# Optimization experiments

Measured on AMD Instinct MI355X. Metric: run time of the kernel, lower is better.

The kernel has to match this reference:

```python
import jax, jax.numpy as jnp
import numpy as np

D_MODEL = 1024
D_STATE = 16
EPS = 1e-5


def _layernorm(x, g, b):
    mu = x.mean(-1, keepdims=True)
    xc = x - mu
    var = (xc * xc).mean(-1, keepdims=True)
    return xc * jax.lax.rsqrt(var + EPS) * g + b


def setup_inputs() -> dict:
    key = jax.random.key(0)
    ks = jax.random.split(key, 10)
    B, L, d, n = 8, 1024, D_MODEL, D_STATE
    s = 1.0 / np.sqrt(d)
    return {
        "x": jax.random.normal(ks[0], (B, L, d), jnp.float32),
        "h_prev": jnp.zeros((B, d * n), jnp.float32),
        "ln_g": jnp.ones((d,), jnp.float32),
        "ln_b": jnp.zeros((d,), jnp.float32),
        "W_ig": jax.random.uniform(ks[1], (2 * d, d), jnp.float32, -s, s),
        "W_dt": jax.random.uniform(ks[2], (d, d), jnp.float32, -s, s),
        "b_dt": jax.random.uniform(ks[3], (d,), jnp.float32, -s, s),
        "A_log": jax.random.uniform(ks[4], (d, n), jnp.float32, -3.0, -1.0),
        "W_B": jax.random.uniform(ks[5], (n, d), jnp.float32, -s, s),
        "W_C": jax.random.uniform(ks[6], (n, d), jnp.float32, -s, s),
        "D": jnp.ones((d,), jnp.float32),
        "W_out": jax.random.uniform(ks[7], (d, d), jnp.float32, -s, s),
    }


def reference(x, h_prev, ln_g, ln_b, W_ig, W_dt, b_dt, A_log, W_B, W_C, D, W_out):
    Bsz, L, d = x.shape
    n = A_log.shape[1]
    x_norm = _layernorm(x, ln_g, ln_b)
    x_proj = jnp.einsum('bld,ed->ble', x_norm, W_ig)  # [B,L,2d]
    x_in, z = x_proj[..., :d], x_proj[..., d:]
    dt = jax.nn.softplus(jnp.einsum('bld,ed->ble', x_in, W_dt) + b_dt)  # [B,L,d]
    A = -jnp.exp(A_log)  # [d,n]
    B_t = jnp.einsum('bld,nd->bln', x_in, W_B)  # [B,L,n]
    C_t = jnp.einsum('bld,nd->bln', x_in, W_C)  # [B,L,n]
    h0 = h_prev.reshape(Bsz, d, n)

    def step(h, inp):
        dt_t, xin_t, Bt_t, Ct_t = inp  # [B,d],[B,d],[B,n],[B,n]
        dA = jnp.exp(dt_t[..., None] * A)                      # [B,d,n]
        h = dA * h + (dt_t * xin_t)[..., None] * Bt_t[:, None, :]
        y_t = (h * Ct_t[:, None, :]).sum(-1)                   # [B,d]
        return h, y_t

    xs = (jnp.swapaxes(dt, 0, 1), jnp.swapaxes(x_in, 0, 1),
          jnp.swapaxes(B_t, 0, 1), jnp.swapaxes(C_t, 0, 1))
    h_final, y = jax.lax.scan(step, h0, xs)
    y = jnp.swapaxes(y, 0, 1)  # [B,L,d]
    ssm_out = y * jax.nn.silu(z) + x_in * D
    out = jnp.einsum('bld,ed->ble', ssm_out, W_out)
    return (x + out, h_final.reshape(Bsz, -1))
```

## Files before the change

kernel.cpp:

```cpp
#include <hip/hip_runtime.h>
#include <hip/hip_bf16.h>
#include <math.h>

#define DM 1024
#define NS 16
#define BSZ 8
#define LSEQ 1024
#define MROWS (BSZ*LSEQ)
#define CH 32

typedef __bf16 bf16;
typedef bf16 bf16x8 __attribute__((ext_vector_type(8)));
typedef bf16 bf16x4 __attribute__((ext_vector_type(4)));
typedef float f32x4 __attribute__((ext_vector_type(4)));
typedef unsigned int u32;
typedef unsigned short u16;

__device__ __forceinline__ void async16(const void* g, void* l) {
  __builtin_amdgcn_global_load_lds((const __attribute__((address_space(1))) void*)g,
                                   (__attribute__((address_space(3))) void*)l,
                                   16, 0, 0);
}

__device__ __forceinline__ float bflo(u32 u) { return __builtin_bit_cast(float, (u32)(u << 16)); }
__device__ __forceinline__ float bfhi(u32 u) { return __builtin_bit_cast(float, (u32)(u & 0xffff0000u)); }

template <int CTRL>
__device__ __forceinline__ float dpp_add(float v) {
  int x = __builtin_amdgcn_update_dpp(0, __builtin_bit_cast(int, v), CTRL, 0xf, 0xf, true);
  return v + __builtin_bit_cast(float, x);
}
__device__ __forceinline__ float row_reduce16(float p) {
  p = dpp_add<0x121>(p);
  p = dpp_add<0x122>(p);
  p = dpp_add<0x124>(p);
  p = dpp_add<0x128>(p);
  return p;
}

__global__ void cast_f2b(const float* __restrict__ s, bf16* __restrict__ d, int n4) {
  int i = blockIdx.x * 256 + threadIdx.x;
  if (i < n4) {
    float4 v = ((const float4*)s)[i];
    bf16x4 o;
    o.x = (bf16)v.x; o.y = (bf16)v.y; o.z = (bf16)v.z; o.w = (bf16)v.w;
    *(bf16x4*)(d + 4 * (size_t)i) = o;
  }
}

__global__ void transpose_cast(const float* __restrict__ src, bf16* __restrict__ dst) {
  __shared__ float tile[64][65];
  const int bk = blockIdx.x * 64;
  const int bd = blockIdx.y * 64;
  const int t = threadIdx.x;
  const int c4 = t & 15;
  const int r0 = t >> 4;
#pragma unroll
  for (int p = 0; p < 4; ++p) {
    int r = r0 + p * 16;
    float4 v = *(const float4*)(src + (size_t)(bd + r) * 1024 + bk + c4 * 4);
    tile[r][c4 * 4 + 0] = v.x;
    tile[r][c4 * 4 + 1] = v.y;
    tile[r][c4 * 4 + 2] = v.z;
    tile[r][c4 * 4 + 3] = v.w;
  }
  __syncthreads();
#pragma unroll
  for (int p = 0; p < 4; ++p) {
    int r = r0 + p * 16;
    bf16x4 o;
    o.x = (bf16)tile[c4 * 4 + 0][r];
    o.y = (bf16)tile[c4 * 4 + 1][r];
    o.z = (bf16)tile[c4 * 4 + 2][r];
    o.w = (bf16)tile[c4 * 4 + 3][r];
    *(bf16x4*)(dst + (size_t)(bk + r) * 1024 + bd + c4 * 4) = o;
  }
}

__global__ void ln_kernel(const float* __restrict__ x, const float* __restrict__ g,
                          const float* __restrict__ b, bf16* __restrict__ out) {
  const size_t row = blockIdx.x;
  const int t = threadIdx.x;
  float4 v = ((const float4*)(x + row * DM))[t];
  float s = v.x + v.y + v.z + v.w;
  float s2 = v.x*v.x + v.y*v.y + v.z*v.z + v.w*v.w;
#pragma unroll
  for (int m = 1; m < 64; m <<= 1) { s += __shfl_xor(s, m, 64); s2 += __shfl_xor(s2, m, 64); }
  __shared__ float red[8];
  int wave = t >> 6, lane = t & 63;
  if (lane == 0) { red[wave] = s; red[4 + wave] = s2; }
  __syncthreads();
  s  = red[0] + red[1] + red[2] + red[3];
  s2 = red[4] + red[5] + red[6] + red[7];
  float mu  = s * (1.f / DM);
  float var = s2 * (1.f / DM) - mu * mu;
  float inv = rsqrtf(var + 1e-5f);
  float4 gg = ((const float4*)g)[t];
  float4 bb = ((const float4*)b)[t];
  bf16x4 o;
  o.x = (bf16)((v.x - mu) * inv * gg.x + bb.x);
  o.y = (bf16)((v.y - mu) * inv * gg.y + bb.y);
  o.z = (bf16)((v.z - mu) * inv * gg.z + bb.z);
  o.w = (bf16)((v.w - mu) * inv * gg.w + bb.w);
  *(bf16x4*)(out + row * DM + t * 4) = o;
}

template <int EPI, bool SWZ>
__global__ __launch_bounds__(256)
void gemm_bf16(const bf16* __restrict__ A, const bf16* __restrict__ W, int K,
               float* __restrict__ out_f, bf16* __restrict__ out_b,
               u16* __restrict__ out_u1, u16* __restrict__ out_u2,
               const float* __restrict__ aux,
               float* __restrict__ out_f3, float* __restrict__ out_f4) {
  __shared__ bf16 As[2][128 * 32];
  __shared__ bf16 Bs[2][128 * 32];
  int tx, ty;
  if (SWZ) {
    int g = blockIdx.x;
    int xcd = g & 7, slot = g >> 3;
    tx = slot >> 3;
    ty = xcd * 8 + (slot & 7);
  } else {
    tx = blockIdx.x; ty = blockIdx.y;
  }
  const int tid  = threadIdx.x;
  const int wave = tid >> 6, lane = tid & 63;
  const int lr = lane & 15, quad = lane >> 4;
  const size_t arow = (size_t)ty * 128;
  const size_t brow = (size_t)tx * 128;
  f32x4 acc[4][4] = {};

  const int srl  = lane >> 2;
  const int kg   = lane & 3;
  const int srow = wave * 32 + srl;
  const int skc  = (kg ^ ((srl >> 1) & 3)) * 8;
  const bf16* ag = A + (arow + srow) * (size_t)K + skc;
  const bf16* wg = W + (brow + srow) * (size_t)K + skc;
  bf16* asl0 = &As[0][wave * 32 * 32];
  bf16* asl1 = &As[1][wave * 32 * 32];
  bf16* bsl0 = &Bs[0][wave * 32 * 32];
  bf16* bsl1 = &Bs[1][wave * 32 * 32];

  const int rk = (quad ^ ((lr >> 1) & 3)) * 8;

  for (int k0 = 0; k0 < K; k0 += 64) {
    async16(ag + k0,                       asl0);
    async16(ag + (size_t)16 * K + k0,      asl0 + 16 * 32);
    async16(ag + k0 + 32,                  asl1);
    async16(ag + (size_t)16 * K + k0 + 32, asl1 + 16 * 32);
    async16(wg + k0,                       bsl0);
    async16(wg + (size_t)16 * K + k0,      bsl0 + 16 * 32);
    async16(wg + k0 + 32,                  bsl1);
    async16(wg + (size_t)16 * K + k0 + 32, bsl1 + 16 * 32);
    __syncthreads();
#pragma unroll
    for (int kh = 0; kh < 2; ++kh) {
      const bf16* ap = &As[kh][(((wave >> 1) * 64) + lr) * 32 + rk];
      const bf16* bp = &Bs[kh][(((wave & 1) * 64) + lr) * 32 + rk];
      bf16x8 af[4], bfr[4];
#pragma unroll
      for (int i = 0; i < 4; ++i) af[i] = *(const bf16x8*)(ap + i * 16 * 32);
#pragma unroll
      for (int j = 0; j < 4; ++j) bfr[j] = *(const bf16x8*)(bp + j * 16 * 32);
#pragma unroll
      for (int i = 0; i < 4; ++i)
#pragma unroll
        for (int j = 0; j < 4; ++j)
          acc[i][j] = __builtin_amdgcn_mfma_f32_16x16x32_bf16(af[i], bfr[j], acc[i][j], 0, 0, 0);
    }
    __syncthreads();
  }

  const size_t mbase = arow + (wave >> 1) * 64;
  const size_t nbase = brow + (wave & 1) * 64;
  if (EPI == 0) {
    if (nbase < DM) {
#pragma unroll
      for (int i = 0; i < 4; ++i)
#pragma unroll
        for (int j = 0; j < 4; ++j)
#pragma unroll
          for (int r = 0; r < 4; ++r) {
            size_t m = mbase + i * 16 + quad * 4 + r;
            size_t n = nbase + j * 16 + lr;
            out_u1[m * DM + n] = __builtin_bit_cast(u16, (bf16)acc[i][j][r]);
          }
    } else if (nbase < 2 * DM) {
#pragma unroll
      for (int i = 0; i < 4; ++i)
#pragma unroll
        for (int j = 0; j < 4; ++j)
#pragma unroll
          for (int r = 0; r < 4; ++r) {
            size_t m = mbase + i * 16 + quad * 4 + r;
            size_t n = nbase - DM + j * 16 + lr;
            out_b[m * DM + n] = (bf16)acc[i][j][r];
          }
    } else if (nbase < 3 * DM) {
#pragma unroll
      for (int i = 0; i < 4; ++i)
#pragma unroll
        for (int j = 0; j < 4; ++j)
#pragma unroll
          for (int r = 0; r < 4; ++r) {
            size_t m = mbase + i * 16 + quad * 4 + r;
            size_t n = nbase - 2 * DM + j * 16 + lr;
            float tt = acc[i][j][r] + aux[n];
            float sp = (tt > 20.f) ? tt : __logf(1.f + __expf(tt));
            out_u2[m * DM + n] = __builtin_bit_cast(u16, (bf16)sp);
          }
    } else if (nbase < 3 * DM + 2 * NS) {
#pragma unroll
      for (int i = 0; i < 4; ++i)
#pragma unroll
        for (int r = 0; r < 4; ++r) {
          size_t m = mbase + i * 16 + quad * 4 + r;
          out_f3[m * NS + lr] = acc[i][0][r];
          out_f4[m * NS + lr] = acc[i][1][r];
        }
    }
  } else {
#pragma unroll
    for (int i = 0; i < 4; ++i)
#pragma unroll
      for (int j = 0; j < 4; ++j)
#pragma unroll
        for (int r = 0; r < 4; ++r) {
          size_t m = mbase + i * 16 + quad * 4 + r;
          size_t n = nbase + j * 16 + lr;
          float v = acc[i][j][r];
          if (EPI == 2) {
            out_f[m * DM + n] = v + aux[m * DM + n];
          } else {
            out_b[m * (size_t)DM + n] = (bf16)v;
          }
        }
  }
}

__global__ __launch_bounds__(256)
void scan_kernel(const u16* __restrict__ dt_b, const u16* __restrict__ xi_b,
                 const bf16* __restrict__ z_b,
                 const float* __restrict__ B_t, const float* __restrict__ C_t,
                 const float* __restrict__ A_log, const float* __restrict__ h_prev,
                 const float* __restrict__ Dvec,
                 bf16* __restrict__ ssm_out, float* __restrict__ h_final) {
  const int blk = blockIdx.x;
  const int b = blk >> 6;
  const int d0 = (blk & 63) * 16;
  const int t = threadIdx.x;
  const int n = t & 15, dl = t >> 4;
  const int d = d0 + dl;
  const float Ac2 = -__expf(A_log[d * NS + n]) * 1.44269504f;
  float h = h_prev[(size_t)b * DM * NS + (size_t)d * NS + n];

  __shared__ u32    dxs[2][CH][16];
  __shared__ float2 bcs[2][CH][16];
  __shared__ float  ys[CH][16];

  const size_t base_row = (size_t)b * LSEQ;
  const int l_a = t >> 4,  c_a = t & 15;
  const int l_b = l_a + 16, c_b = c_a;
  const float Dva = Dvec[d0 + c_a];

  float za, zb;
  {
    size_t ga = (base_row + l_a) * DM + d0 + c_a;
    size_t gb = (base_row + l_b) * DM + d0 + c_b;
    dxs[0][l_a][c_a] = (u32)dt_b[ga] | ((u32)xi_b[ga] << 16);
    dxs[0][l_b][c_b] = (u32)dt_b[gb] | ((u32)xi_b[gb] << 16);
    za = (float)z_b[ga]; zb = (float)z_b[gb];
    size_t gB = base_row * NS;
    bcs[0][l_a][c_a] = make_float2(B_t[gB + t],       C_t[gB + t]);
    bcs[0][l_b][c_b] = make_float2(B_t[gB + t + 256], C_t[gB + t + 256]);
  }
  __syncthreads();

  for (int c = 0; c < LSEQ / CH; ++c) {
    const int cur = c & 1, nxt = cur ^ 1;
    u32 pdxa, pdxb; float2 pbca, pbcb; float pza, pzb;
    if (c + 1 < LSEQ / CH) {
      size_t l0 = (size_t)(c + 1) * CH;
      size_t ga = (base_row + l0 + l_a) * DM + d0 + c_a;
      size_t gb = (base_row + l0 + l_b) * DM + d0 + c_b;
      pdxa = (u32)dt_b[ga] | ((u32)xi_b[ga] << 16);
      pdxb = (u32)dt_b[gb] | ((u32)xi_b[gb] << 16);
      pza = (float)z_b[ga]; pzb = (float)z_b[gb];
      size_t gB = (base_row + l0) * NS;
      pbca = make_float2(B_t[gB + t],       C_t[gB + t]);
      pbcb = make_float2(B_t[gB + t + 256], C_t[gB + t + 256]);
    }
#pragma unroll
    for (int l = 0; l < CH; ++l) {
      u32 u = dxs[cur][l][dl];
      float dtv = bflo(u), xiv = bfhi(u);
      float2 bc = bcs[cur][l][n];
      float a = __builtin_amdgcn_exp2f(dtv * Ac2);
      h = fmaf(a, h, (dtv * xiv) * bc.x);
      float p = row_reduce16(h * bc.y);
      if (n == 0) ys[l][dl] = p;
    }
    __syncthreads();
    {
      size_t l0 = (size_t)c * CH;
      float xa = bfhi(dxs[cur][l_a][c_a]);
      float xb = bfhi(dxs[cur][l_b][c_b]);
      float sa = za / (1.f + __expf(-za));
      float sb = zb / (1.f + __expf(-zb));
      ssm_out[(base_row + l0 + l_a) * DM + d0 + c_a] = (bf16)(ys[l_a][c_a] * sa + xa * Dva);
      ssm_out[(base_row + l0 + l_b) * DM + d0 + c_b] = (bf16)(ys[l_b][c_b] * sb + xb * Dva);
    }
    if (c + 1 < LSEQ / CH) {
      dxs[nxt][l_a][c_a] = pdxa;
      dxs[nxt][l_b][c_b] = pdxb;
      bcs[nxt][l_a][c_a] = pbca;
      bcs[nxt][l_b][c_b] = pbcb;
      za = pza; zb = pzb;
    }
    __syncthreads();
  }
  h_final[(size_t)b * DM * NS + (size_t)d0 * NS + t] = h;
}

extern "C" void kernel_launch(void* const* d_in, const int* in_sizes, int n_in,
                              void* d_out, int out_size, void* d_ws, size_t ws_size,
                              hipStream_t stream) {
  const float* x      = (const float*)d_in[0];
  const float* h_prev = (const float*)d_in[1];
  const float* ln_g   = (const float*)d_in[2];
  const float* ln_b   = (const float*)d_in[3];
  const float* W_ig   = (const float*)d_in[4];
  const float* W_dt   = (const float*)d_in[5];
  const float* b_dt   = (const float*)d_in[6];
  const float* A_log  = (const float*)d_in[7];
  const float* W_B    = (const float*)d_in[8];
  const float* W_C    = (const float*)d_in[9];
  const float* Dvec   = (const float*)d_in[10];
  const float* W_out  = (const float*)d_in[11];

  char* ws = (char*)d_ws;
  size_t off = 0;
  auto alloc = [&](size_t bytes) -> char* {
    char* p = ws + off;
    off += (bytes + 255) & ~(size_t)255;
    return p;
  };
  bf16*  wmega_b = (bf16*)alloc((size_t)3200 * DM * 2);
  bf16*  wstack_b= (bf16*)alloc((size_t)1152 * DM * 2);
  bf16*  wigT_b  = (bf16*)alloc((size_t)DM * DM * 2);
  bf16*  wout_b  = (bf16*)alloc((size_t)DM * DM * 2);
  bf16*  xnorm_b = (bf16*)alloc((size_t)MROWS * DM * 2);
  u16*   xi_w    = (u16*)alloc((size_t)MROWS * DM * 2);
  u16*   dt_w    = (u16*)alloc((size_t)MROWS * DM * 2);
  bf16*  z_bb    = (bf16*)alloc((size_t)MROWS * DM * 2);
  bf16*  ssm_b   = (bf16*)alloc((size_t)MROWS * DM * 2);
  float* Bt      = (float*)alloc((size_t)MROWS * NS * 4);
  float* Ct      = (float*)alloc((size_t)MROWS * NS * 4);
  (void)ws_size; (void)in_sizes; (void)n_in; (void)out_size;

  float* out_main = (float*)d_out;
  float* out_h    = (float*)d_out + (size_t)MROWS * DM;

  cast_f2b<<<(2 * DM * DM / 4 + 255) / 256, 256, 0, stream>>>(W_ig, wmega_b, 2 * DM * DM / 4);
  cast_f2b<<<(DM * DM / 4 + 255) / 256, 256, 0, stream>>>(W_dt, wstack_b, DM * DM / 4);
  cast_f2b<<<(NS * DM / 4 + 255) / 256, 256, 0, stream>>>(W_B, wstack_b + (size_t)DM * DM, NS * DM / 4);
  cast_f2b<<<(NS * DM / 4 + 255) / 256, 256, 0, stream>>>(W_C, wstack_b + (size_t)(DM + NS) * DM, NS * DM / 4);
  cast_f2b<<<(DM * DM / 4 + 255) / 256, 256, 0, stream>>>(W_out, wout_b, DM * DM / 4);
  transpose_cast<<<dim3(16, 16), 256, 0, stream>>>(W_ig, wigT_b);

  ln_kernel<<<MROWS, 256, 0, stream>>>(x, ln_g, ln_b, xnorm_b);

  gemm_bf16<3, false><<<dim3(8, 9), 256, 0, stream>>>(wstack_b, wigT_b, DM,
      nullptr, wmega_b + (size_t)2048 * DM, nullptr, nullptr, nullptr, nullptr, nullptr);

  gemm_bf16<0, true><<<1600, 256, 0, stream>>>(xnorm_b, wmega_b, DM,
      nullptr, z_bb, xi_w, dt_w, b_dt, Bt, Ct);

  scan_kernel<<<512, 256, 0, stream>>>(dt_w, xi_w, z_bb, Bt, Ct, A_log, h_prev,
                                       Dvec, ssm_b, out_h);

  gemm_bf16<2, true><<<512, 256, 0, stream>>>(ssm_b, wout_b, DM,
      out_main, nullptr, nullptr, nullptr, x, nullptr, nullptr);
}
```

Before: 375.9 us.

## Transpose scan LDS layout for vector loads and defer C-reduction out of recurrence

The scan kernel now stores dt/x, B and C transposed in padded LDS rows so each thread reads four timesteps with one 128-bit load. The per-step 16-lane DPP reduction of h*C is replaced by writing the partial products to a padded LDS buffer, which is summed after the chunk. This takes the cross-lane reduction off the serial recurrence critical path and cuts the number of LDS read instructions. In exchange it adds about 34KB of LDS traffic per chunk and more shared memory per block, which may lower occupancy.

Measured after the change: 345.0 us. -8.2%, faster.

```diff
diff --git a/kernel.cpp b/kernel.cpp
--- a/kernel.cpp
+++ b/kernel.cpp
@@ -8,6 +8,7 @@
 #define LSEQ 1024
 #define MROWS (BSZ*LSEQ)
 #define CH 32
+#define ROWP 36
 
 typedef __bf16 bf16;
 typedef bf16 bf16x8 __attribute__((ext_vector_type(8)));
@@ -15,6 +16,7 @@
 typedef float f32x4 __attribute__((ext_vector_type(4)));
 typedef unsigned int u32;
 typedef unsigned short u16;
+typedef u32 u32x4 __attribute__((ext_vector_type(4)));
 
 __device__ __forceinline__ void async16(const void* g, void* l) {
   __builtin_amdgcn_global_load_lds((const __attribute__((address_space(1))) void*)g,
@@ -24,19 +26,6 @@
 
 __device__ __forceinline__ float bflo(u32 u) { return __builtin_bit_cast(float, (u32)(u << 16)); }
 __device__ __forceinline__ float bfhi(u32 u) { return __builtin_bit_cast(float, (u32)(u & 0xffff0000u)); }
-
-template <int CTRL>
-__device__ __forceinline__ float dpp_add(float v) {
-  int x = __builtin_amdgcn_update_dpp(0, __builtin_bit_cast(int, v), CTRL, 0xf, 0xf, true);
-  return v + __builtin_bit_cast(float, x);
-}
-__device__ __forceinline__ float row_reduce16(float p) {
-  p = dpp_add<0x121>(p);
-  p = dpp_add<0x122>(p);
-  p = dpp_add<0x124>(p);
-  p = dpp_add<0x128>(p);
-  return p;
-}
 
 __global__ void cast_f2b(const float* __restrict__ s, bf16* __restrict__ d, int n4) {
   int i = blockIdx.x * 256 + threadIdx.x;
@@ -254,67 +243,80 @@
   const float Ac2 = -__expf(A_log[d * NS + n]) * 1.44269504f;
   float h = h_prev[(size_t)b * DM * NS + (size_t)d * NS + n];
 
-  __shared__ u32    dxs[2][CH][16];
-  __shared__ float2 bcs[2][CH][16];
-  __shared__ float  ys[CH][16];
+  __shared__ u32   dxs[2][16][ROWP];
+  __shared__ float Bsh[2][16][ROWP];
+  __shared__ float Csh[2][16][ROWP];
+  __shared__ float ys_p[CH][16][17];
 
   const size_t base_row = (size_t)b * LSEQ;
-  const int l_a = t >> 4,  c_a = t & 15;
-  const int l_b = l_a + 16, c_b = c_a;
+  const int l_a = t >> 4, c_a = t & 15;
   const float Dva = Dvec[d0 + c_a];
 
-  float za, zb;
   {
     size_t ga = (base_row + l_a) * DM + d0 + c_a;
-    size_t gb = (base_row + l_b) * DM + d0 + c_b;
-    dxs[0][l_a][c_a] = (u32)dt_b[ga] | ((u32)xi_b[ga] << 16);
-    dxs[0][l_b][c_b] = (u32)dt_b[gb] | ((u32)xi_b[gb] << 16);
-    za = (float)z_b[ga]; zb = (float)z_b[gb];
+    size_t gb = (base_row + l_a + 16) * DM + d0 + c_a;
+    dxs[0][c_a][l_a]      = (u32)dt_b[ga] | ((u32)xi_b[ga] << 16);
+    dxs[0][c_a][l_a + 16] = (u32)dt_b[gb] | ((u32)xi_b[gb] << 16);
     size_t gB = base_row * NS;
-    bcs[0][l_a][c_a] = make_float2(B_t[gB + t],       C_t[gB + t]);
-    bcs[0][l_b][c_b] = make_float2(B_t[gB + t + 256], C_t[gB + t + 256]);
-  }
+    Bsh[0][c_a][l_a]      = B_t[gB + t];
+    Csh[0][c_a][l_a]      = C_t[gB + t];
+    Bsh[0][c_a][l_a + 16] = B_t[gB + t + 256];
+    Csh[0][c_a][l_a + 16] = C_t[gB + t + 256];
+  }
+  float za = (float)z_b[(base_row + l_a) * DM + d0 + c_a];
+  float zb = (float)z_b[(base_row + l_a + 16) * DM + d0 + c_a];
   __syncthreads();
 
   for (int c = 0; c < LSEQ / CH; ++c) {
     const int cur = c & 1, nxt = cur ^ 1;
-    u32 pdxa, pdxb; float2 pbca, pbcb; float pza, pzb;
+    u32 pdxa, pdxb; float pBa, pBb, pCa, pCb, pza, pzb;
     if (c + 1 < LSEQ / CH) {
       size_t l0 = (size_t)(c + 1) * CH;
       size_t ga = (base_row + l0 + l_a) * DM + d0 + c_a;
-      size_t gb = (base_row + l0 + l_b) * DM + d0 + c_b;
+      size_t gb = (base_row + l0 + l_a + 16) * DM + d0 + c_a;
       pdxa = (u32)dt_b[ga] | ((u32)xi_b[ga] << 16);
       pdxb = (u32)dt_b[gb] | ((u32)xi_b[gb] << 16);
       pza = (float)z_b[ga]; pzb = (float)z_b[gb];
       size_t gB = (base_row + l0) * NS;
-      pbca = make_float2(B_t[gB + t],       C_t[gB + t]);
-      pbcb = make_float2(B_t[gB + t + 256], C_t[gB + t + 256]);
-    }
-#pragma unroll
-    for (int l = 0; l < CH; ++l) {
-      u32 u = dxs[cur][l][dl];
-      float dtv = bflo(u), xiv = bfhi(u);
-      float2 bc = bcs[cur][l][n];
-      float a = __builtin_amdgcn_exp2f(dtv * Ac2);
-      h = fmaf(a, h, (dtv * xiv) * bc.x);
-      float p = row_reduce16(h * bc.y);
-      if (n == 0) ys[l][dl] = p;
+      pBa = B_t[gB + t];       pCa = C_t[gB + t];
+      pBb = B_t[gB + t + 256]; pCb = C_t[gB + t + 256];
+    }
+#pragma unroll
+    for (int l4 = 0; l4 < CH; l4 += 4) {
+      u32x4 dx4 = *(const u32x4*)&dxs[cur][dl][l4];
+      f32x4 b4  = *(const f32x4*)&Bsh[cur][n][l4];
+      f32x4 c4  = *(const f32x4*)&Csh[cur][n][l4];
+#pragma unroll
+      for (int i = 0; i < 4; ++i) {
+        float dtv = bflo(dx4[i]), xiv = bfhi(dx4[i]);
+        float a = __builtin_amdgcn_exp2f(dtv * Ac2);
+        h = fmaf(a, h, (dtv * xiv) * b4[i]);
+        ys_p[l4 + i][dl][n] = h * c4[i];
+      }
     }
     __syncthreads();
     {
+      float s1 = 0.f, s2 = 0.f;
+#pragma unroll
+      for (int k = 0; k < 16; ++k) {
+        s1 += ys_p[l_a][c_a][k];
+        s2 += ys_p[l_a + 16][c_a][k];
+      }
+      float x1 = bfhi(dxs[cur][c_a][l_a]);
+      float x2 = bfhi(dxs[cur][c_a][l_a + 16]);
+      float g1 = za / (1.f + __expf(-za));
+      float g2 = zb / (1.f + __expf(-zb));
       size_t l0 = (size_t)c * CH;
-      float xa = bfhi(dxs[cur][l_a][c_a]);
-      float xb = bfhi(dxs[cur][l_b][c_b]);
-      float sa = za / (1.f + __expf(-za));
-      float sb = zb / (1.f + __expf(-zb));
-      ssm_out[(base_row + l0 + l_a) * DM + d0 + c_a] = (bf16)(ys[l_a][c_a] * sa + xa * Dva);
-      ssm_out[(base_row + l0 + l_b) * DM + d0 + c_b] = (bf16)(ys[l_b][c_b] * sb + xb * Dva);
+      ssm_out[(base_row + l0 + l_a) * DM + d0 + c_a]      = (bf16)(s1 * g1 + x1 * Dva);
+      ssm_out[(base_row + l0 + l_a + 16) * DM + d0 + c_a] = (bf16)(s2 * g2 + x2 * Dva);
     }
     if (c + 1 < LSEQ / CH) {
-      dxs[nxt][l_a][c_a] = pdxa;
-      dxs[nxt][l_b][c_b] = pdxb;
-      bcs[nxt][l_a][c_a] = pbca;
-      bcs[nxt][l_b][c_b] = pbcb;
+      dxs[nxt][c_a][l_a]      = pdxa;
+      dxs[nxt][c_a][l_a + 16] = pdxb;
+      Bsh[nxt][c_a][l_a]      = pBa;
+      Csh[nxt][c_a][l_a]      = pCa;
+      Bsh[nxt][c_a][l_a + 16] = pBb;
+      Csh[nxt][c_a][l_a + 16] = pCb;
       za = pza; zb = pzb;
     }
     __syncthreads();
```

## Split sequential scan into segmented two-pass scan with carry combine

Applied to the files above, without the earlier changes.

Replaces the single sequential scan over 1024 steps (512 blocks) with a chunked scan: pass 1 computes each segment's end state and decay product, a combine kernel propagates carries across the 8 segments, and pass 2 recomputes each segment from its start state to produce outputs. This exposes 8x more blocks to fill the GPU and shortens the serial dependency chain. In exchange it reads the inputs twice, recomputes the exponentials, adds two extra launches and writes intermediate state buffers. It also moves to transposed LDS layouts with vectorized reads and an XCD-aware block mapping.

Result: faster. 359.5 us (-4.4%).

```diff
diff --git a/kernel.cpp b/kernel.cpp
--- a/kernel.cpp
+++ b/kernel.cpp
@@ -7,7 +7,9 @@
 #define BSZ 8
 #define LSEQ 1024
 #define MROWS (BSZ*LSEQ)
-#define CH 32
+#define NSEG 8
+#define SEGL (LSEQ/NSEG)
+#define ROWP 132
 
 typedef __bf16 bf16;
 typedef bf16 bf16x8 __attribute__((ext_vector_type(8)));
@@ -15,6 +17,7 @@
 typedef float f32x4 __attribute__((ext_vector_type(4)));
 typedef unsigned int u32;
 typedef unsigned short u16;
+typedef u32 u32x4 __attribute__((ext_vector_type(4)));
 
 __device__ __forceinline__ void async16(const void* g, void* l) {
   __builtin_amdgcn_global_load_lds((const __attribute__((address_space(1))) void*)g,
@@ -36,6 +39,13 @@
   p = dpp_add<0x124>(p);
   p = dpp_add<0x128>(p);
   return p;
+}
+
+__device__ __forceinline__ void seg_decode(int blk, int& s, int& b, int& d0) {
+  int xcd = blk & 7, rest = blk >> 3;
+  int q0 = rest & 3, q1 = (rest >> 2) & 1, sb = rest >> 3;
+  int dgrp = q0 | (xcd << 2) | (q1 << 5);
+  s = sb >> 3; b = sb & 7; d0 = dgrp * 16;
 }
 
 __global__ void cast_f2b(const float* __restrict__ s, bf16* __restrict__ d, int n4) {
@@ -239,87 +249,135 @@
 }
 
 __global__ __launch_bounds__(256)
-void scan_kernel(const u16* __restrict__ dt_b, const u16* __restrict__ xi_b,
-                 const bf16* __restrict__ z_b,
-                 const float* __restrict__ B_t, const float* __restrict__ C_t,
-                 const float* __restrict__ A_log, const float* __restrict__ h_prev,
-                 const float* __restrict__ Dvec,
-                 bf16* __restrict__ ssm_out, float* __restrict__ h_final) {
-  const int blk = blockIdx.x;
-  const int b = blk >> 6;
-  const int d0 = (blk & 63) * 16;
+void scan_pass1(const u16* __restrict__ dt_b, const u16* __restrict__ xi_b,
+                const float* __restrict__ B_t, const float* __restrict__ A_log,
+                float* __restrict__ hend, float* __restrict__ pprod) {
+  int s, b, d0; seg_decode(blockIdx.x, s, b, d0);
   const int t = threadIdx.x;
   const int n = t & 15, dl = t >> 4;
-  const int d = d0 + dl;
-  const float Ac2 = -__expf(A_log[d * NS + n]) * 1.44269504f;
-  float h = h_prev[(size_t)b * DM * NS + (size_t)d * NS + n];
-
-  __shared__ u32    dxs[2][CH][16];
-  __shared__ float2 bcs[2][CH][16];
-  __shared__ float  ys[CH][16];
-
-  const size_t base_row = (size_t)b * LSEQ;
-  const int l_a = t >> 4,  c_a = t & 15;
-  const int l_b = l_a + 16, c_b = c_a;
+  const float Ac2 = -__expf(A_log[(d0 + dl) * NS + n]) * 1.44269504f;
+
+  __shared__ u32   dxs[16][ROWP];
+  __shared__ float Bsh[16][ROWP];
+
+  const size_t base_row = (size_t)b * LSEQ + (size_t)s * SEGL;
+  const int l_a = t >> 4, c_a = t & 15;
+#pragma unroll
+  for (int k = 0; k < 8; ++k) {
+    int l = l_a + 16 * k;
+    size_t ga = (base_row + l) * DM + d0 + c_a;
+    dxs[c_a][l] = (u32)dt_b[ga] | ((u32)xi_b[ga] << 16);
+  }
+#pragma unroll
+  for (int k = 0; k < 2; ++k) {
+    int idx = t + 256 * k;
+    int l = idx >> 2, j4 = (idx & 3) * 4;
+    float4 v = *(const float4*)(B_t + (base_row + l) * NS + j4);
+    Bsh[j4 + 0][l] = v.x; Bsh[j4 + 1][l] = v.y;
+    Bsh[j4 + 2][l] = v.z; Bsh[j4 + 3][l] = v.w;
+  }
+  __syncthreads();
+
+  float h = 0.f, P = 1.f;
+#pragma unroll 4
+  for (int l4 = 0; l4 < SEGL; l4 += 4) {
+    u32x4 dx4 = *(const u32x4*)&dxs[dl][l4];
+    f32x4 b4  = *(const f32x4*)&Bsh[n][l4];
+#pragma unroll
+    for (int i = 0; i < 4; ++i) {
+      float dtv = bflo(dx4[i]), xiv = bfhi(dx4[i]);
+      float a = __builtin_amdgcn_exp2f(dtv * Ac2);
+      h = fmaf(a, h, (dtv * xiv) * b4[i]);
+      P *= a;
+    }
+  }
+  size_t idx = ((size_t)(s * 8 + b)) * (DM * NS) + d0 * 16 + t;
+  hend[idx] = h;
+  pprod[idx] = P;
+}
+
+__global__ void scan_combine(const float* __restrict__ h_prev,
+                             const float* __restrict__ hend,
+                             const float* __restrict__ pprod,
+                             float* __restrict__ hstart,
+                             float* __restrict__ h_final) {
+  size_t gid = (size_t)blockIdx.x * 256 + threadIdx.x;
+  int b = (int)(gid >> 14);
+  size_t j = gid & 16383;
+  float hs = h_prev[gid];
+#pragma unroll
+  for (int s = 0; s < NSEG; ++s) {
+    size_t idx = ((size_t)(s * 8 + b)) * (DM * NS) + j;
+    hstart[idx] = hs;
+    hs = fmaf(pprod[idx], hs, hend[idx]);
+  }
+  h_final[gid] = hs;
+}
+
+__global__ __launch_bounds__(256)
+void scan_pass2(const u16* __restrict__ dt_b, const u16* __restrict__ xi_b,
+                const bf16* __restrict__ z_b,
+                const float* __restrict__ B_t, const float* __restrict__ C_t,
+                const float* __restrict__ A_log, const float* __restrict__ hstart,
+                const float* __restrict__ Dvec, bf16* __restrict__ ssm_out) {
+  int s, b, d0; seg_decode(blockIdx.x, s, b, d0);
+  const int t = threadIdx.x;
+  const int n = t & 15, dl = t >> 4;
+  const float Ac2 = -__expf(A_log[(d0 + dl) * NS + n]) * 1.44269504f;
+
+  __shared__ u32   dxs[16][ROWP];
+  __shared__ float Bsh[16][ROWP];
+  __shared__ float Csh[16][ROWP];
+  __shared__ float ys[SEGL][17];
+
+  const size_t base_row = (size_t)b * LSEQ + (size_t)s * SEGL;
+  const int l_a = t >> 4, c_a = t & 15;
+#pragma unroll
+  for (int k = 0; k < 8; ++k) {
+    int l = l_a + 16 * k;
+    size_t ga = (base_row + l) * DM + d0 + c_a;
+    dxs[c_a][l] = (u32)dt_b[ga] | ((u32)xi_b[ga] << 16);
+  }
+#pragma unroll
+  for (int k = 0; k < 2; ++k) {
+    int idx = t + 256 * k;
+    int l = idx >> 2, j4 = (idx & 3) * 4;
+    float4 v = *(const float4*)(B_t + (base_row + l) * NS + j4);
+    Bsh[j4 + 0][l] = v.x; Bsh[j4 + 1][l] = v.y;
+    Bsh[j4 + 2][l] = v.z; Bsh[j4 + 3][l] = v.w;
+    float4 w = *(const float4*)(C_t + (base_row + l) * NS + j4);
+    Csh[j4 + 0][l] = w.x; Csh[j4 + 1][l] = w.y;
+    Csh[j4 + 2][l] = w.z; Csh[j4 + 3][l] = w.w;
+  }
+  float h = hstart[((size_t)(s * 8 + b)) * (DM * NS) + d0 * 16 + t];
+  __syncthreads();
+
+#pragma unroll 4
+  for (int l4 = 0; l4 < SEGL; l4 += 4) {
+    u32x4 dx4 = *(const u32x4*)&dxs[dl][l4];
+    f32x4 b4  = *(const f32x4*)&Bsh[n][l4];
+    f32x4 c4  = *(const f32x4*)&Csh[n][l4];
+#pragma unroll
+    for (int i = 0; i < 4; ++i) {
+      float dtv = bflo(dx4[i]), xiv = bfhi(dx4[i]);
+      float a = __builtin_amdgcn_exp2f(dtv * Ac2);
+      h = fmaf(a, h, (dtv * xiv) * b4[i]);
+      float p = row_reduce16(h * c4[i]);
+      if (n == 0) ys[l4 + i][dl] = p;
+    }
+  }
+  __syncthreads();
+
   const float Dva = Dvec[d0 + c_a];
-
-  float za, zb;
-  {
-    size_t ga = (base_row + l_a) * DM + d0 + c_a;
-    size_t gb = (base_row + l_b) * DM + d0 + c_b;
-    dxs[0][l_a][c_a] = (u32)dt_b[ga] | ((u32)xi_b[ga] << 16);
-    dxs[0][l_b][c_b] = (u32)dt_b[gb] | ((u32)xi_b[gb] << 16);
-    za = (float)z_b[ga]; zb = (float)z_b[gb];
-    size_t gB = base_row * NS;
-    bcs[0][l_a][c_a] = make_float2(B_t[gB + t],       C_t[gB + t]);
-    bcs[0][l_b][c_b] = make_float2(B_t[gB + t + 256], C_t[gB + t + 256]);
-  }
-  __syncthreads();
-
-  for (int c = 0; c < LSEQ / CH; ++c) {
-    const int cur = c & 1, nxt = cur ^ 1;
-    u32 pdxa, pdxb; float2 pbca, pbcb; float pza, pzb;
-    if (c + 1 < LSEQ / CH) {
-      size_t l0 = (size_t)(c + 1) * CH;
-      size_t ga = (base_row + l0 + l_a) * DM + d0 + c_a;
-      size_t gb = (base_row + l0 + l_b) * DM + d0 + c_b;
-      pdxa = (u32)dt_b[ga] | ((u32)xi_b[ga] << 16);
-      pdxb = (u32)dt_b[gb] | ((u32)xi_b[gb] << 16);
-      pza = (float)z_b[ga]; pzb = (float)z_b[gb];
-      size_t gB = (base_row + l0) * NS;
-      pbca = make_float2(B_t[gB + t],       C_t[gB + t]);
-      pbcb = make_float2(B_t[gB + t + 256], C_t[gB + t + 256]);
-    }
-#pragma unroll
-    for (int l = 0; l < CH; ++l) {
-      u32 u = dxs[cur][l][dl];
-      float dtv = bflo(u), xiv = bfhi(u);
-      float2 bc = bcs[cur][l][n];
-      float a = __builtin_amdgcn_exp2f(dtv * Ac2);
-      h = fmaf(a, h, (dtv * xiv) * bc.x);
-      float p = row_reduce16(h * bc.y);
-      if (n == 0) ys[l][dl] = p;
-    }
-    __syncthreads();
-    {
-      size_t l0 = (size_t)c * CH;
-      float xa = bfhi(dxs[cur][l_a][c_a]);
-      float xb = bfhi(dxs[cur][l_b][c_b]);
-      float sa = za / (1.f + __expf(-za));
-      float sb = zb / (1.f + __expf(-zb));
-      ssm_out[(base_row + l0 + l_a) * DM + d0 + c_a] = (bf16)(ys[l_a][c_a] * sa + xa * Dva);
-      ssm_out[(base_row + l0 + l_b) * DM + d0 + c_b] = (bf16)(ys[l_b][c_b] * sb + xb * Dva);
-    }
-    if (c + 1 < LSEQ / CH) {
-      dxs[nxt][l_a][c_a] = pdxa;
-      dxs[nxt][l_b][c_b] = pdxb;
-      bcs[nxt][l_a][c_a] = pbca;
-      bcs[nxt][l_b][c_b] = pbcb;
-      za = pza; zb = pzb;
-    }
-    __syncthreads();
-  }
-  h_final[(size_t)b * DM * NS + (size_t)d0 * NS + t] = h;
+#pragma unroll
+  for (int k = 0; k < 8; ++k) {
+    int l = l_a + 16 * k;
+    size_t grow = base_row + l;
+    float zv = (float)z_b[grow * DM + d0 + c_a];
+    float gate = zv / (1.f + __expf(-zv));
+    float xi = bfhi(dxs[c_a][l]);
+    ssm_out[grow * DM + d0 + c_a] = (bf16)(ys[l][c_a] * gate + xi * Dva);
+  }
 }
 
 extern "C" void kernel_launch(void* const* d_in, const int* in_sizes, int n_in,
@@ -356,6 +414,9 @@
   bf16*  ssm_b   = (bf16*)alloc((size_t)MROWS * DM * 2);
   float* Bt      = (float*)alloc((size_t)MROWS * NS * 4);
   float* Ct      = (float*)alloc((size_t)MROWS * NS * 4);
+  float* hend_w  = (float*)alloc((size_t)NSEG * DM * NS * BSZ * 4);
+  float* pprod_w = (float*)alloc((size_t)NSEG * DM * NS * BSZ * 4);
+  float* hstart_w= (float*)alloc((size_t)NSEG * DM * NS * BSZ * 4);
   (void)ws_size; (void)in_sizes; (void)n_in; (void)out_size;
 
   float* out_main = (float*)d_out;
@@ -376,8 +437,10 @@
   gemm_bf16<0, true><<<1600, 256, 0, stream>>>(xnorm_b, wmega_b, DM,
       nullptr, z_bb, xi_w, dt_w, b_dt, Bt, Ct);
 
-  scan_kernel<<<512, 256, 0, stream>>>(dt_w, xi_w, z_bb, Bt, Ct, A_log, h_prev,
-                                       Dvec, ssm_b, out_h);
+  scan_pass1<<<4096, 256, 0, stream>>>(dt_w, xi_w, Bt, A_log, hend_w, pprod_w);
+  scan_combine<<<512, 256, 0, stream>>>(h_prev, hend_w, pprod_w, hstart_w, out_h);
+  scan_pass2<<<4096, 256, 0, stream>>>(dt_w, xi_w, z_bb, Bt, Ct, A_log,
+                                       hstart_w, Dvec, ssm_b);
 
   gemm_bf16<2, true><<<512, 256, 0, stream>>>(ssm_b, wout_b, DM,
       out_main, nullptr, nullptr, nullptr, x, nullptr, nullptr);
```
